# Performance work log

Measured on AMD Instinct MI355X. Metric: run time of the kernel, lower is better.

The kernel has to match this reference:

```python
import jax, jax.numpy as jnp
import numpy as np
import math

CAPACITY_FACTOR = 1.0

def setup_inputs() -> dict:
    key = jax.random.key(0)
    k1, k2 = jax.random.split(key)
    x = jax.random.normal(k1, (8192, 2048), dtype=jnp.float32)
    wg = jax.random.normal(k2, (64, 2048), dtype=jnp.float32) * (1.0 / np.sqrt(2048))
    return {"x": x, "wg": wg}

def reference(x, wg):
    # logits = Linear(model_dim, num_experts, bias=False)(x)
    logits = jnp.einsum('sd,ed->se', x, wg)
    gates = jax.nn.softmax(logits, axis=1)  # [s, e]
    s, e = gates.shape
    capacity = math.ceil(s / e * CAPACITY_FACTOR)  # static
    indices1_s = jnp.argmax(gates, axis=1)  # [s]
    mask1 = jax.nn.one_hot(indices1_s, e, dtype=jnp.int32)  # [s, e]
    locations1 = jnp.cumsum(mask1, axis=0) - 1  # position within each expert queue
    # aux load-balancing loss
    me = jnp.mean(gates, axis=0)
    ce = jnp.mean(mask1.astype(gates.dtype), axis=0)
    l_aux = jnp.mean(me * ce) * (e * e)
    # drop tokens over capacity
    mask1 = mask1 * (locations1 < capacity).astype(jnp.int32)
    locations1_s = jnp.sum(locations1 * mask1, axis=1)  # [s] int
    mask1_float = mask1.astype(gates.dtype)
    gates1_s = jnp.sum(gates * mask1_float, axis=1)  # 'se,se->s'
    gates1 = gates1_s[:, None] * mask1_float         # 's,se->se'
    locations1_sc = jax.nn.one_hot(locations1_s, capacity, dtype=gates.dtype)  # [s, c]
    combine_weights = gates1[:, :, None] * locations1_sc[:, None, :]  # 'se,sc->sec'
    dispatch_mask = combine_weights.astype(bool)
    return l_aux, combine_weights, dispatch_mask
```

## Files before the change

kernel.cpp:

```cpp
#include <hip/hip_runtime.h>
#include <cstdint>
#include <cstddef>


#define S_TOK 8192
#define NEXP 64
#define DIM 2048
#define CAP 128
#define COMB_ELEMS ((size_t)S_TOK * NEXP * CAP)
#define OUT_ELEMS (1 + 2 * COMB_ELEMS)
#define NQUAD ((size_t)(OUT_ELEMS / 4))

#define QA ((size_t)14000000)
#define QB ((size_t)24000000)

#define TOK_TILE 128
#define NSLICE 4
#define KSLICE (DIM / NSLICE)
#define KC 32

__device__ __forceinline__ void zero_quads(float* __restrict__ out,
                                           size_t q_begin, size_t q_end,
                                           int nblocks, int bid) {
    const float4 z = { 0.0f, 0.0f, 0.0f, 0.0f };
    size_t stride = (size_t)nblocks * blockDim.x;
    for (size_t q = q_begin + (size_t)bid * blockDim.x + threadIdx.x;
         q < q_end; q += stride)
        *(float4*)(out + 4 * q) = z;
}

__global__ __launch_bounds__(256, 4) void gemm_zero_a(
    const float* __restrict__ x, const float* __restrict__ wg,
    float* __restrict__ P, float* __restrict__ gsum,
    float* __restrict__ out)
{
    const int tid = threadIdx.x;

    if (blockIdx.x >= 256) {
        const int zb = blockIdx.x - 256;
        zero_quads(out, 0, QA, 768, zb);
        if (zb == 0 && tid == 0) out[OUT_ELEMS - 1] = 0.0f;
        return;
    }

    __shared__ float xs[KC][132];
    __shared__ float wsh[KC][68];

    const int tile  = blockIdx.x >> 2;
    const int slice = blockIdx.x & 3;
    const int tok0 = tile * TOK_TILE;
    const int k0   = slice * KSLICE;

    if (blockIdx.x == 0 && tid < NEXP) gsum[tid] = 0.0f;

    const int tt = tid >> 4;
    const int te = tid & 15;

    float acc[8][4];
#pragma unroll
    for (int i = 0; i < 8; ++i)
#pragma unroll
        for (int j = 0; j < 4; ++j) acc[i][j] = 0.0f;

    const int we  = tid & 63;
    const int wkq = tid >> 6;

    float4 xv[4], wv[2];
#pragma unroll
    for (int r = 0; r < 4; ++r) {
        int idx = tid + 256 * r;
        int t = idx >> 3, kq = idx & 7;
        xv[r] = *(const float4*)(x + (size_t)(tok0 + t) * DIM + k0 + 4 * kq);
    }
    wv[0] = *(const float4*)(wg + (size_t)we * DIM + k0 + 4 * wkq);
    wv[1] = *(const float4*)(wg + (size_t)we * DIM + k0 + 4 * (wkq + 4));

    for (int kc = 0; kc < KSLICE; kc += KC) {
        __syncthreads();
#pragma unroll
        for (int r = 0; r < 4; ++r) {
            int idx = tid + 256 * r;
            int t = idx >> 3, k4 = (idx & 7) * 4;
            xs[k4 + 0][t] = xv[r].x; xs[k4 + 1][t] = xv[r].y;
            xs[k4 + 2][t] = xv[r].z; xs[k4 + 3][t] = xv[r].w;
        }
        {
            int k4 = 4 * wkq;
            wsh[k4 + 0][we] = wv[0].x; wsh[k4 + 1][we] = wv[0].y;
            wsh[k4 + 2][we] = wv[0].z; wsh[k4 + 3][we] = wv[0].w;
            int k4b = k4 + 16;
            wsh[k4b + 0][we] = wv[1].x; wsh[k4b + 1][we] = wv[1].y;
            wsh[k4b + 2][we] = wv[1].z; wsh[k4b + 3][we] = wv[1].w;
        }
        __syncthreads();
        if (kc + KC < KSLICE) {
#pragma unroll
            for (int r = 0; r < 4; ++r) {
                int idx = tid + 256 * r;
                int t = idx >> 3, kq = idx & 7;
                xv[r] = *(const float4*)(x + (size_t)(tok0 + t) * DIM + k0 + kc + KC + 4 * kq);
            }
            wv[0] = *(const float4*)(wg + (size_t)we * DIM + k0 + kc + KC + 4 * wkq);
            wv[1] = *(const float4*)(wg + (size_t)we * DIM + k0 + kc + KC + 4 * (wkq + 4));
        }
#pragma unroll 8
        for (int k = 0; k < KC; ++k) {
            float4 a0 = *(const float4*)&xs[k][8 * tt];
            float4 a1 = *(const float4*)&xs[k][8 * tt + 4];
            float4 b  = *(const float4*)&wsh[k][4 * te];
            const float* ap0 = &a0.x; const float* ap1 = &a1.x; const float* bp = &b.x;
#pragma unroll
            for (int i = 0; i < 4; ++i)
#pragma unroll
                for (int j = 0; j < 4; ++j) {
                    acc[i][j]     += ap0[i] * bp[j];
                    acc[i + 4][j] += ap1[i] * bp[j];
                }
        }
    }

#pragma unroll
    for (int i = 0; i < 8; ++i) {
        size_t off = ((size_t)slice * S_TOK + tok0 + 8 * tt + i) * NEXP + 4 * te;
        float4 v = { acc[i][0], acc[i][1], acc[i][2], acc[i][3] };
        *(float4*)(P + off) = v;
    }
}

__global__ __launch_bounds__(256) void reduce_zero_b(
    const float* __restrict__ P,
    int* __restrict__ idx_out, float* __restrict__ gate_out,
    float* __restrict__ gsum, float* __restrict__ out)
{
    const int tid = threadIdx.x;

    if (blockIdx.x >= 256) {
        zero_quads(out, QA, QB, 768, blockIdx.x - 256);
        return;
    }

    __shared__ float sme[NEXP];
    const int tok0 = blockIdx.x * 32;
    const int ty = tid >> 5;
    const int tx = tid & 31;
    const int t0 = ty * 4;
    const int e0 = tx * 2;

    if (tid < NEXP) sme[tid] = 0.0f;

    float gm0 = 0.0f, gm1 = 0.0f;
#pragma unroll
    for (int i = 0; i < 4; ++i) {
        int tok = tok0 + t0 + i;
        float l0 = 0.0f, l1 = 0.0f;
#pragma unroll
        for (int s = 0; s < NSLICE; ++s) {
            float2 p = *(const float2*)&P[((size_t)s * S_TOK + tok) * NEXP + e0];
            l0 += p.x; l1 += p.y;
        }
        float v; int ix;
        if (l1 > l0) { v = l1; ix = e0 + 1; } else { v = l0; ix = e0; }
#pragma unroll
        for (int off = 16; off; off >>= 1) {
            float ov = __shfl_xor(v, off, 32);
            int   oi = __shfl_xor(ix, off, 32);
            if (ov > v || (ov == v && oi < ix)) { v = ov; ix = oi; }
        }
        float z0 = __expf(l0 - v), z1 = __expf(l1 - v);
        float zs = z0 + z1;
#pragma unroll
        for (int off = 16; off; off >>= 1) zs += __shfl_xor(zs, off, 32);
        float inv = 1.0f / zs;
        gm0 += z0 * inv; gm1 += z1 * inv;
        if (tx == 0) {
            idx_out[tok]  = ix;
            gate_out[tok] = inv;
        }
    }
    atomicAdd(&sme[e0], gm0);
    atomicAdd(&sme[e0 + 1], gm1);
    __syncthreads();
    if (tid < NEXP) atomicAdd(&gsum[tid], sme[tid]);
}

__global__ __launch_bounds__(1024) void scan_zero_c(
    const int* __restrict__ idx, const float* __restrict__ gsum,
    int* __restrict__ loc_out, float* __restrict__ out)
{
    const int tid = threadIdx.x;

    if (blockIdx.x > 0) {
        zero_quads(out, QB, NQUAD, 256, (int)blockIdx.x - 1);
        return;
    }

    __shared__ int wavecnt[16][NEXP];
    __shared__ int basecnt[NEXP];
    const int lane = tid & 63;
    const int wv   = tid >> 6;

    if (tid < NEXP) basecnt[tid] = 0;
    __syncthreads();

    for (int it = 0; it < S_TOK / 1024; ++it) {
        int tok = it * 1024 + tid;
        int e = idx[tok];
        unsigned long long m = ~0ull, lm = ~0ull;
#pragma unroll
        for (int b = 0; b < 6; ++b) {
            unsigned long long bal = __ballot((e >> b) & 1);
            m  &= ((e >> b) & 1)    ? bal : ~bal;
            lm &= ((lane >> b) & 1) ? bal : ~bal;
        }
        int rank = __popcll(m & ((1ull << lane) - 1ull));
        wavecnt[wv][lane] = __popcll(lm);
        __syncthreads();
        int off = 0;
        for (int w = 0; w < wv; ++w) off += wavecnt[w][e];
        loc_out[tok] = basecnt[e] + off + rank;
        __syncthreads();
        if (tid < NEXP) {
            int tot = 0;
#pragma unroll
            for (int w = 0; w < 16; ++w) tot += wavecnt[w][tid];
            basecnt[tid] += tot;
        }
        __syncthreads();
    }

    if (tid < NEXP) {
        float p = gsum[tid] * (float)basecnt[tid];
#pragma unroll
        for (int off = 32; off; off >>= 1) p += __shfl_xor(p, off, 64);
        if (tid == 0) out[0] = p * 9.5367431640625e-07f;
    }
}

__global__ __launch_bounds__(256) void scatter_kernel(
    const int* __restrict__ idx, const float* __restrict__ gate,
    const int* __restrict__ loc, float* __restrict__ out)
{
    int t = blockIdx.x * 256 + threadIdx.x;
    int l = loc[t];
    if (l < CAP) {
        size_t base = 1 + (size_t)t * (NEXP * CAP) + (size_t)idx[t] * CAP + l;
        out[base] = gate[t];
        out[base + COMB_ELEMS] = 1.0f;
    }
}

extern "C" void kernel_launch(void* const* d_in, const int* in_sizes, int n_in,
                              void* d_out, int out_size, void* d_ws, size_t ws_size,
                              hipStream_t stream) {
    const float* x  = (const float*)d_in[0];
    const float* wg = (const float*)d_in[1];
    float* out = (float*)d_out;

    int*   idx  = (int*)d_ws;
    float* gate = (float*)((char*)d_ws + 32768);
    float* gsum = (float*)((char*)d_ws + 65536);
    int*   loc  = (int*)((char*)d_ws + 66560);
    float* P    = (float*)((char*)d_ws + 262144);

    gemm_zero_a<<<1024, 256, 0, stream>>>(x, wg, P, gsum, out);
    reduce_zero_b<<<1024, 256, 0, stream>>>(P, idx, gate, gsum, out);
    scan_zero_c<<<257, 1024, 0, stream>>>(idx, gsum, loc, out);
    scatter_kernel<<<S_TOK / 256, 256, 0, stream>>>(idx, gate, loc, out);
}
```

Measured before the change: 590.9 us.

## Fuse reduce and scan kernels using a global arrival counter

Merges the reduce/softmax kernel and the serial scan kernel into one launch. Block 0 spin-waits on a global atomic counter until all 256 reduce blocks finish, then runs the location scan with 256 threads while the remaining blocks zero the output. The output zeroing is rebalanced across the two remaining kernels. This removes one kernel launch and its boundary bubble, and overlaps the serial scan with the bulk zeroing. It risks a deadlock if block 0 becomes resident before the reduce blocks can be scheduled. The scan also runs with a smaller block, so it takes more iterations.

```diff
diff --git a/kernel.cpp b/kernel.cpp
--- a/kernel.cpp
+++ b/kernel.cpp
@@ -11,8 +11,7 @@
 #define OUT_ELEMS (1 + 2 * COMB_ELEMS)
 #define NQUAD ((size_t)(OUT_ELEMS / 4))
 
-#define QA ((size_t)14000000)
-#define QB ((size_t)24000000)
+#define QA ((size_t)14800000)
 
 #define TOK_TILE 128
 #define NSLICE 4
@@ -32,14 +31,17 @@
 __global__ __launch_bounds__(256, 4) void gemm_zero_a(
     const float* __restrict__ x, const float* __restrict__ wg,
     float* __restrict__ P, float* __restrict__ gsum,
-    float* __restrict__ out)
+    int* __restrict__ ctr, float* __restrict__ out)
 {
     const int tid = threadIdx.x;
 
     if (blockIdx.x >= 256) {
         const int zb = blockIdx.x - 256;
         zero_quads(out, 0, QA, 768, zb);
-        if (zb == 0 && tid == 0) out[OUT_ELEMS - 1] = 0.0f;
+        if (zb == 0 && tid == 0) {
+            out[OUT_ELEMS - 1] = 0.0f;
+            *ctr = 0;
+        }
         return;
     }
 
@@ -127,26 +129,78 @@
     }
 }
 
-__global__ __launch_bounds__(256) void reduce_zero_b(
+__global__ __launch_bounds__(256) void reduce_scan_zero(
     const float* __restrict__ P,
     int* __restrict__ idx_out, float* __restrict__ gate_out,
-    float* __restrict__ gsum, float* __restrict__ out)
+    float* __restrict__ gsum, int* __restrict__ loc_out,
+    int* __restrict__ ctr, float* __restrict__ out)
 {
     const int tid = threadIdx.x;
 
-    if (blockIdx.x >= 256) {
-        zero_quads(out, QA, QB, 768, blockIdx.x - 256);
+    if (blockIdx.x >= 257) {
+        zero_quads(out, QA, NQUAD, 768, blockIdx.x - 257);
         return;
     }
 
+    if (blockIdx.x == 0) {
+        if (tid == 0) {
+            while (atomicAdd(ctr, 0) < 256) __builtin_amdgcn_s_sleep(2);
+        }
+        __syncthreads();
+        __threadfence();
+
+        __shared__ int wavecnt[4][NEXP];
+        __shared__ int basecnt[NEXP];
+        const int lane = tid & 63;
+        const int wv   = tid >> 6;
+
+        if (tid < NEXP) basecnt[tid] = 0;
+        __syncthreads();
+
+        for (int it = 0; it < S_TOK / 256; ++it) {
+            int tok = it * 256 + tid;
+            int e = idx_out[tok];
+            unsigned long long m = ~0ull, lm = ~0ull;
+#pragma unroll
+            for (int b = 0; b < 6; ++b) {
+                unsigned long long bal = __ballot((e >> b) & 1);
+                m  &= ((e >> b) & 1)    ? bal : ~bal;
+                lm &= ((lane >> b) & 1) ? bal : ~bal;
+            }
+            int rank = __popcll(m & ((1ull << lane) - 1ull));
+            wavecnt[wv][lane] = __popcll(lm);
+            __syncthreads();
+            int off = 0;
+            for (int w = 0; w < wv; ++w) off += wavecnt[w][e];
+            loc_out[tok] = basecnt[e] + off + rank;
+            __syncthreads();
+            if (tid < NEXP) {
+                int tot = 0;
+#pragma unroll
+                for (int w = 0; w < 4; ++w) tot += wavecnt[w][tid];
+                basecnt[tid] += tot;
+            }
+            __syncthreads();
+        }
+
+        if (tid < NEXP) {
+            float p = gsum[tid] * (float)basecnt[tid];
+#pragma unroll
+            for (int off = 32; off; off >>= 1) p += __shfl_xor(p, off, 64);
+            if (tid == 0) out[0] = p * 9.5367431640625e-07f;
+        }
+        return;
+    }
+
     __shared__ float sme[NEXP];
-    const int tok0 = blockIdx.x * 32;
+    const int tok0 = (blockIdx.x - 1) * 32;
     const int ty = tid >> 5;
     const int tx = tid & 31;
     const int t0 = ty * 4;
     const int e0 = tx * 2;
 
     if (tid < NEXP) sme[tid] = 0.0f;
+    __syncthreads();
 
     float gm0 = 0.0f, gm1 = 0.0f;
 #pragma unroll
@@ -181,59 +235,10 @@
     atomicAdd(&sme[e0 + 1], gm1);
     __syncthreads();
     if (tid < NEXP) atomicAdd(&gsum[tid], sme[tid]);
-}
-
-__global__ __launch_bounds__(1024) void scan_zero_c(
-    const int* __restrict__ idx, const float* __restrict__ gsum,
-    int* __restrict__ loc_out, float* __restrict__ out)
-{
-    const int tid = threadIdx.x;
-
-    if (blockIdx.x > 0) {
-        zero_quads(out, QB, NQUAD, 256, (int)blockIdx.x - 1);
-        return;
-    }
-
-    __shared__ int wavecnt[16][NEXP];
-    __shared__ int basecnt[NEXP];
-    const int lane = tid & 63;
-    const int wv   = tid >> 6;
-
-    if (tid < NEXP) basecnt[tid] = 0;
+
+    __threadfence();
     __syncthreads();
-
-    for (int it = 0; it < S_TOK / 1024; ++it) {
-        int tok = it * 1024 + tid;
-        int e = idx[tok];
-        unsigned long long m = ~0ull, lm = ~0ull;
-#pragma unroll
-        for (int b = 0; b < 6; ++b) {
-            unsigned long long bal = __ballot((e >> b) & 1);
-            m  &= ((e >> b) & 1)    ? bal : ~bal;
-            lm &= ((lane >> b) & 1) ? bal : ~bal;
-        }
-        int rank = __popcll(m & ((1ull << lane) - 1ull));
-        wavecnt[wv][lane] = __popcll(lm);
-        __syncthreads();
-        int off = 0;
-        for (int w = 0; w < wv; ++w) off += wavecnt[w][e];
-        loc_out[tok] = basecnt[e] + off + rank;
-        __syncthreads();
-        if (tid < NEXP) {
-            int tot = 0;
-#pragma unroll
-            for (int w = 0; w < 16; ++w) tot += wavecnt[w][tid];
-            basecnt[tid] += tot;
-        }
-        __syncthreads();
-    }
-
-    if (tid < NEXP) {
-        float p = gsum[tid] * (float)basecnt[tid];
-#pragma unroll
-        for (int off = 32; off; off >>= 1) p += __shfl_xor(p, off, 64);
-        if (tid == 0) out[0] = p * 9.5367431640625e-07f;
-    }
+    if (tid == 0) atomicAdd(ctr, 1);
 }
 
 __global__ __launch_bounds__(256) void scatter_kernel(
@@ -259,11 +264,11 @@
     int*   idx  = (int*)d_ws;
     float* gate = (float*)((char*)d_ws + 32768);
     float* gsum = (float*)((char*)d_ws + 65536);
+    int*   ctr  = (int*)((char*)d_ws + 65792);
     int*   loc  = (int*)((char*)d_ws + 66560);
     float* P    = (float*)((char*)d_ws + 262144);
 
-    gemm_zero_a<<<1024, 256, 0, stream>>>(x, wg, P, gsum, out);
-    reduce_zero_b<<<1024, 256, 0, stream>>>(P, idx, gate, gsum, out);
-    scan_zero_c<<<257, 1024, 0, stream>>>(idx, gsum, loc, out);
+    gemm_zero_a<<<1024, 256, 0, stream>>>(x, wg, P, gsum, ctr, out);
+    reduce_scan_zero<<<1025, 256, 0, stream>>>(P, idx, gate, gsum, loc, ctr, out);
     scatter_kernel<<<S_TOK / 256, 256, 0, stream>>>(idx, gate, loc, out);
 }
```

Result: slower. 627.6 us (+6.2%).

## Fuse gating GEMM with softmax/argmax and drop split-K partial buffer

Applied to the files above, without the earlier changes.

The gating GEMM now gives each block 32 full tokens over the whole K dimension instead of split-K tiles of 128 tokens, so softmax, argmax, gate and per-block expert-sum partials are computed in the same kernel. This removes the partial-logit buffer round trip, the separate reduce kernel and the global atomics on gsum. The scan kernel reduces the per-block gate partials deterministically and takes on a larger share of the output zeroing with more blocks. The cost is less register tiling per thread (2x4 instead of 8x4), which lowers the arithmetic reuse of the GEMM, and a different split of the zero-fill between kernels.

```diff
diff --git a/kernel.cpp b/kernel.cpp
--- a/kernel.cpp
+++ b/kernel.cpp
@@ -11,13 +11,13 @@
 #define OUT_ELEMS (1 + 2 * COMB_ELEMS)
 #define NQUAD ((size_t)(OUT_ELEMS / 4))
 
-#define QA ((size_t)14000000)
-#define QB ((size_t)24000000)
-
-#define TOK_TILE 128
+#define QA ((size_t)14777216)
+
+#define TOK_TILE 32
 #define NSLICE 4
 #define KSLICE (DIM / NSLICE)
 #define KC 32
+#define NCHUNK (DIM / KC)
 
 __device__ __forceinline__ void zero_quads(float* __restrict__ out,
                                            size_t q_begin, size_t q_end,
@@ -29,10 +29,10 @@
         *(float4*)(out + 4 * q) = z;
 }
 
-__global__ __launch_bounds__(256, 4) void gemm_zero_a(
+__global__ __launch_bounds__(256, 4) void gemm_softmax_zero_a(
     const float* __restrict__ x, const float* __restrict__ wg,
-    float* __restrict__ P, float* __restrict__ gsum,
-    float* __restrict__ out)
+    int* __restrict__ idx_out, float* __restrict__ gate_out,
+    float* __restrict__ gpart, float* __restrict__ out)
 {
     const int tid = threadIdx.x;
 
@@ -43,159 +43,115 @@
         return;
     }
 
-    __shared__ float xs[KC][132];
+    __shared__ float xs[KC][34];
     __shared__ float wsh[KC][68];
-
-    const int tile  = blockIdx.x >> 2;
-    const int slice = blockIdx.x & 3;
-    const int tok0 = tile * TOK_TILE;
-    const int k0   = slice * KSLICE;
-
-    if (blockIdx.x == 0 && tid < NEXP) gsum[tid] = 0.0f;
-
+    __shared__ float sme[NEXP];
+
+    const int tok0 = blockIdx.x * TOK_TILE;
     const int tt = tid >> 4;
     const int te = tid & 15;
 
-    float acc[8][4];
-#pragma unroll
-    for (int i = 0; i < 8; ++i)
-#pragma unroll
-        for (int j = 0; j < 4; ++j) acc[i][j] = 0.0f;
-
-    const int we  = tid & 63;
-    const int wkq = tid >> 6;
-
-    float4 xv[4], wv[2];
-#pragma unroll
-    for (int r = 0; r < 4; ++r) {
-        int idx = tid + 256 * r;
-        int t = idx >> 3, kq = idx & 7;
-        xv[r] = *(const float4*)(x + (size_t)(tok0 + t) * DIM + k0 + 4 * kq);
-    }
-    wv[0] = *(const float4*)(wg + (size_t)we * DIM + k0 + 4 * wkq);
-    wv[1] = *(const float4*)(wg + (size_t)we * DIM + k0 + 4 * (wkq + 4));
-
-    for (int kc = 0; kc < KSLICE; kc += KC) {
-        __syncthreads();
-#pragma unroll
-        for (int r = 0; r < 4; ++r) {
-            int idx = tid + 256 * r;
-            int t = idx >> 3, k4 = (idx & 7) * 4;
-            xs[k4 + 0][t] = xv[r].x; xs[k4 + 1][t] = xv[r].y;
-            xs[k4 + 2][t] = xv[r].z; xs[k4 + 3][t] = xv[r].w;
-        }
-        {
-            int k4 = 4 * wkq;
-            wsh[k4 + 0][we] = wv[0].x; wsh[k4 + 1][we] = wv[0].y;
-            wsh[k4 + 2][we] = wv[0].z; wsh[k4 + 3][we] = wv[0].w;
-            int k4b = k4 + 16;
-            wsh[k4b + 0][we] = wv[1].x; wsh[k4b + 1][we] = wv[1].y;
-            wsh[k4b + 2][we] = wv[1].z; wsh[k4b + 3][we] = wv[1].w;
-        }
-        __syncthreads();
-        if (kc + KC < KSLICE) {
-#pragma unroll
-            for (int r = 0; r < 4; ++r) {
-                int idx = tid + 256 * r;
-                int t = idx >> 3, kq = idx & 7;
-                xv[r] = *(const float4*)(x + (size_t)(tok0 + t) * DIM + k0 + kc + KC + 4 * kq);
+    const int xt = tid >> 3;
+    const int xk = tid & 7;
+    const int es = tid >> 3;
+
+    float l[8];
+#pragma unroll
+    for (int o = 0; o < 8; ++o) l[o] = 0.0f;
+
+    float4 xv  = *(const float4*)(x  + (size_t)(tok0 + xt) * DIM + 4 * xk);
+    float4 wv0 = *(const float4*)(wg + (size_t)es * DIM + 4 * xk);
+    float4 wv1 = *(const float4*)(wg + (size_t)(es + 32) * DIM + 4 * xk);
+
+#pragma unroll
+    for (int s = 0; s < NSLICE; ++s) {
+        float acc[8];
+#pragma unroll
+        for (int o = 0; o < 8; ++o) acc[o] = 0.0f;
+
+        for (int kci = 0; kci < KSLICE / KC; ++kci) {
+            const int c = s * (KSLICE / KC) + kci;
+            __syncthreads();
+            xs[4 * xk + 0][xt] = xv.x; xs[4 * xk + 1][xt] = xv.y;
+            xs[4 * xk + 2][xt] = xv.z; xs[4 * xk + 3][xt] = xv.w;
+            wsh[4 * xk + 0][es] = wv0.x; wsh[4 * xk + 1][es] = wv0.y;
+            wsh[4 * xk + 2][es] = wv0.z; wsh[4 * xk + 3][es] = wv0.w;
+            wsh[4 * xk + 0][es + 32] = wv1.x; wsh[4 * xk + 1][es + 32] = wv1.y;
+            wsh[4 * xk + 2][es + 32] = wv1.z; wsh[4 * xk + 3][es + 32] = wv1.w;
+            __syncthreads();
+            if (c + 1 < NCHUNK) {
+                const int kb = KC * (c + 1);
+                xv  = *(const float4*)(x  + (size_t)(tok0 + xt) * DIM + kb + 4 * xk);
+                wv0 = *(const float4*)(wg + (size_t)es * DIM + kb + 4 * xk);
+                wv1 = *(const float4*)(wg + (size_t)(es + 32) * DIM + kb + 4 * xk);
             }
-            wv[0] = *(const float4*)(wg + (size_t)we * DIM + k0 + kc + KC + 4 * wkq);
-            wv[1] = *(const float4*)(wg + (size_t)we * DIM + k0 + kc + KC + 4 * (wkq + 4));
-        }
 #pragma unroll 8
-        for (int k = 0; k < KC; ++k) {
-            float4 a0 = *(const float4*)&xs[k][8 * tt];
-            float4 a1 = *(const float4*)&xs[k][8 * tt + 4];
-            float4 b  = *(const float4*)&wsh[k][4 * te];
-            const float* ap0 = &a0.x; const float* ap1 = &a1.x; const float* bp = &b.x;
-#pragma unroll
-            for (int i = 0; i < 4; ++i)
+            for (int k = 0; k < KC; ++k) {
+                float2 a = *(const float2*)&xs[k][2 * tt];
+                float4 b = *(const float4*)&wsh[k][4 * te];
+                const float* bp = &b.x;
 #pragma unroll
                 for (int j = 0; j < 4; ++j) {
-                    acc[i][j]     += ap0[i] * bp[j];
-                    acc[i + 4][j] += ap1[i] * bp[j];
+                    acc[j]     += a.x * bp[j];
+                    acc[4 + j] += a.y * bp[j];
                 }
-        }
-    }
-
-#pragma unroll
-    for (int i = 0; i < 8; ++i) {
-        size_t off = ((size_t)slice * S_TOK + tok0 + 8 * tt + i) * NEXP + 4 * te;
-        float4 v = { acc[i][0], acc[i][1], acc[i][2], acc[i][3] };
-        *(float4*)(P + off) = v;
-    }
-}
-
-__global__ __launch_bounds__(256) void reduce_zero_b(
-    const float* __restrict__ P,
-    int* __restrict__ idx_out, float* __restrict__ gate_out,
-    float* __restrict__ gsum, float* __restrict__ out)
-{
-    const int tid = threadIdx.x;
-
-    if (blockIdx.x >= 256) {
-        zero_quads(out, QA, QB, 768, blockIdx.x - 256);
-        return;
-    }
-
-    __shared__ float sme[NEXP];
-    const int tok0 = blockIdx.x * 32;
-    const int ty = tid >> 5;
-    const int tx = tid & 31;
-    const int t0 = ty * 4;
-    const int e0 = tx * 2;
+            }
+        }
+#pragma unroll
+        for (int o = 0; o < 8; ++o) l[o] += acc[o];
+    }
 
     if (tid < NEXP) sme[tid] = 0.0f;
-
-    float gm0 = 0.0f, gm1 = 0.0f;
-#pragma unroll
-    for (int i = 0; i < 4; ++i) {
-        int tok = tok0 + t0 + i;
-        float l0 = 0.0f, l1 = 0.0f;
-#pragma unroll
-        for (int s = 0; s < NSLICE; ++s) {
-            float2 p = *(const float2*)&P[((size_t)s * S_TOK + tok) * NEXP + e0];
-            l0 += p.x; l1 += p.y;
-        }
-        float v; int ix;
-        if (l1 > l0) { v = l1; ix = e0 + 1; } else { v = l0; ix = e0; }
-#pragma unroll
-        for (int off = 16; off; off >>= 1) {
-            float ov = __shfl_xor(v, off, 32);
-            int   oi = __shfl_xor(ix, off, 32);
+    __syncthreads();
+
+#pragma unroll
+    for (int g = 0; g < 2; ++g) {
+        const float l0 = l[4 * g + 0], l1 = l[4 * g + 1];
+        const float l2 = l[4 * g + 2], l3 = l[4 * g + 3];
+        float v = l0; int ix = 4 * te;
+        if (l1 > v) { v = l1; ix = 4 * te + 1; }
+        if (l2 > v) { v = l2; ix = 4 * te + 2; }
+        if (l3 > v) { v = l3; ix = 4 * te + 3; }
+#pragma unroll
+        for (int off = 8; off; off >>= 1) {
+            float ov = __shfl_xor(v, off, 16);
+            int   oi = __shfl_xor(ix, off, 16);
             if (ov > v || (ov == v && oi < ix)) { v = ov; ix = oi; }
         }
         float z0 = __expf(l0 - v), z1 = __expf(l1 - v);
-        float zs = z0 + z1;
-#pragma unroll
-        for (int off = 16; off; off >>= 1) zs += __shfl_xor(zs, off, 32);
-        float inv = 1.0f / zs;
-        gm0 += z0 * inv; gm1 += z1 * inv;
-        if (tx == 0) {
+        float z2 = __expf(l2 - v), z3 = __expf(l3 - v);
+        float zs = ((z0 + z1) + z2) + z3;
+#pragma unroll
+        for (int off = 8; off; off >>= 1) zs += __shfl_xor(zs, off, 16);
+        const float inv = 1.0f / zs;
+        const int tok = tok0 + 2 * tt + g;
+        if (te == 0) {
             idx_out[tok]  = ix;
             gate_out[tok] = inv;
         }
-    }
-    atomicAdd(&sme[e0], gm0);
-    atomicAdd(&sme[e0 + 1], gm1);
-    __syncthreads();
-    if (tid < NEXP) atomicAdd(&gsum[tid], sme[tid]);
-}
-
-__global__ __launch_bounds__(1024) void scan_zero_c(
-    const int* __restrict__ idx, const float* __restrict__ gsum,
+        atomicAdd(&sme[4 * te + 0], z0 * inv);
+        atomicAdd(&sme[4 * te + 1], z1 * inv);
+        atomicAdd(&sme[4 * te + 2], z2 * inv);
+        atomicAdd(&sme[4 * te + 3], z3 * inv);
+    }
+    __syncthreads();
+    if (tid < NEXP) gpart[(size_t)blockIdx.x * NEXP + tid] = sme[tid];
+}
+
+__global__ __launch_bounds__(1024) void scan_zero_b(
+    const int* __restrict__ idx, const float* __restrict__ gpart,
     int* __restrict__ loc_out, float* __restrict__ out)
 {
     const int tid = threadIdx.x;
 
     if (blockIdx.x > 0) {
-        zero_quads(out, QB, NQUAD, 256, (int)blockIdx.x - 1);
+        zero_quads(out, QA, NQUAD, 511, (int)blockIdx.x - 1);
         return;
     }
 
-    __shared__ int wavecnt[16][NEXP];
-    __shared__ int basecnt[NEXP];
+    __shared__ int   wavecnt[16][NEXP];
+    __shared__ int   basecnt[NEXP];
+    __shared__ float fsum[16][NEXP];
     const int lane = tid & 63;
     const int wv   = tid >> 6;
 
@@ -228,8 +184,19 @@
         __syncthreads();
     }
 
+    {
+        float g = 0.0f;
+#pragma unroll
+        for (int r = 0; r < 16; ++r)
+            g += gpart[(size_t)(wv * 16 + r) * NEXP + lane];
+        fsum[wv][lane] = g;
+    }
+    __syncthreads();
     if (tid < NEXP) {
-        float p = gsum[tid] * (float)basecnt[tid];
+        float g = 0.0f;
+#pragma unroll
+        for (int w = 0; w < 16; ++w) g += fsum[w][tid];
+        float p = g * (float)basecnt[tid];
 #pragma unroll
         for (int off = 32; off; off >>= 1) p += __shfl_xor(p, off, 64);
         if (tid == 0) out[0] = p * 9.5367431640625e-07f;
@@ -256,14 +223,12 @@
     const float* wg = (const float*)d_in[1];
     float* out = (float*)d_out;
 
-    int*   idx  = (int*)d_ws;
-    float* gate = (float*)((char*)d_ws + 32768);
-    float* gsum = (float*)((char*)d_ws + 65536);
-    int*   loc  = (int*)((char*)d_ws + 66560);
-    float* P    = (float*)((char*)d_ws + 262144);
-
-    gemm_zero_a<<<1024, 256, 0, stream>>>(x, wg, P, gsum, out);
-    reduce_zero_b<<<1024, 256, 0, stream>>>(P, idx, gate, gsum, out);
-    scan_zero_c<<<257, 1024, 0, stream>>>(idx, gsum, loc, out);
+    int*   idx   = (int*)d_ws;
+    float* gate  = (float*)((char*)d_ws + 32768);
+    int*   loc   = (int*)((char*)d_ws + 65536);
+    float* gpart = (float*)((char*)d_ws + 131072);
+
+    gemm_softmax_zero_a<<<1024, 256, 0, stream>>>(x, wg, idx, gate, gpart, out);
+    scan_zero_b<<<512, 1024, 0, stream>>>(idx, gpart, loc, out);
     scatter_kernel<<<S_TOK / 256, 256, 0, stream>>>(idx, gate, loc, out);
 }
```

New measurement: 615.2 us. +4.1%, slower.
